# Kernel tuning notes

Measured on AMD Instinct MI355X. Metric: run time of the kernel, lower is better.

Reference implementation:

```python
import jax, jax.numpy as jnp
import numpy as np

B, N, F, D, TOPK, EXTRA = 32, 128, 10, 64, 20, 25
BN = B * N
EPS = 1e-5
SLOPE = 0.2  # GDN GraphLayer leaky_relu negative slope


def _cosine(a, b):
    na = jnp.maximum(jnp.linalg.norm(a, axis=-1), 1e-12)
    nb = jnp.maximum(jnp.linalg.norm(b, axis=-1), 1e-12)
    return (a @ b.T) / (na[:, None] * nb[None, :])


def _segment_softmax(logits, seg, num):
    m = jax.ops.segment_max(logits, seg, num_segments=num)
    m = jnp.where(jnp.isfinite(m), m, 0.0)  # empty segments
    e = jnp.exp(logits - m[seg])
    s = jax.ops.segment_sum(e, seg, num_segments=num)
    return e / jnp.maximum(s[seg], 1e-12)


def setup_inputs() -> dict:
    key = jax.random.key(0)
    ks = jax.random.split(key, 12)
    r = lambda i, shape, s=1.0: jax.random.normal(ks[i], shape, dtype=jnp.float32) * s
    return dict(
        data=r(0, (B, N, F)),
        emb=r(1, (N, D)) * 0.3,                       # nn.Embedding(node_num, dim)
        W1=r(2, (F, D)) * (1.0 / np.sqrt(F)),         # GraphLayer lin
        att_i1=r(3, (2 * D,)) * 0.1,                  # att on concat(h, emb)
        att_j1=r(4, (2 * D,)) * 0.1,
        bias1=jnp.zeros((D,), jnp.float32),
        bn1_g=jnp.ones((D,), jnp.float32),
        bn1_b=jnp.zeros((D,), jnp.float32),
        P=r(5, (BN, BN)) * (1.0 / np.sqrt(BN)),       # extra_pram
        W2=r(6, (D, D)) * (1.0 / np.sqrt(D)),         # GraphLayer1 lin
        att_i2=r(7, (D,)) * 0.1,
        att_j2=r(8, (D,)) * 0.1,
        bias2=jnp.zeros((D,), jnp.float32),
        bnO_g=jnp.ones((D,), jnp.float32),
        bnO_b=jnp.zeros((D,), jnp.float32),
        W_out=r(9, (D, 1)) * (1.0 / np.sqrt(D)),      # OutLayer Linear(dim,1)
        b_out=jnp.zeros((1,), jnp.float32),
        org_edge_index=jnp.zeros((2, 2), jnp.int32),  # dead arg in original forward
    )


def _forward(data, emb, W1, att_i1, att_j1, bias1, bn1_g, bn1_b, P, W2,
             att_i2, att_j2, bias2, bnO_g, bnO_b, W_out, b_out):
    x = data.reshape(BN, F)

    # ---- learned top-k graph from detached embedding cosine similarity ----
    w = jax.lax.stop_gradient(emb)              # weights_arr = detach()
    cos = _cosine(w, w)                         # [N, N]
    topv, topi = jax.lax.top_k(cos, TOPK)       # [N, TOPK]
    cos_w = jnp.tile(topv.reshape(-1), B)       # [B*N*TOPK]
    src0 = topi.reshape(-1)                     # gated_j (source)
    dst0 = jnp.repeat(jnp.arange(N), TOPK)      # gated_i (target)
    offs = jnp.repeat(jnp.arange(B) * N, N * TOPK)
    src = jnp.tile(src0, B) + offs
    dst = jnp.tile(dst0, B) + offs

    # ---- GraphLayer (GAT-style with embedding keys, edge weight = cos) ----
    all_emb = jnp.tile(emb, (B, 1))             # [BN, D]
    h = x @ W1                                  # [BN, D]
    kf = jnp.concatenate([h, all_emb], axis=-1) # [BN, 2D]
    si, sj = kf @ att_i1, kf @ att_j1           # [BN]
    score = jax.nn.leaky_relu(si[dst] + sj[src], SLOPE) * cos_w
    alpha = _segment_softmax(score, dst, BN)
    agg = jax.ops.segment_sum(h[src] * alpha[:, None], dst, num_segments=BN) + bias1
    mu, var = agg.mean(0), agg.var(0)           # BatchNorm1d (batch stats)
    gcn = jax.nn.relu(bn1_g * (agg - mu) / jnp.sqrt(var + EPS) + bn1_b)

    # ---- extra-feature branch (always taken: P is [BN, BN]) ----
    ef = P.T @ gcn                              # (gcn_out.T @ P).T
    g = jnp.concatenate([gcn, ef], axis=0)      # [2BN, D]
    cos2 = _cosine(g, g)                        # [2BN, 2BN]
    topv2, topi2 = jax.lax.top_k(cos2, EXTRA)
    corrs = topv2[:BN].reshape(-1)              # [BN*EXTRA]
    src2 = jnp.repeat(jnp.arange(BN), EXTRA)    # extra_i = edge_index[0] (source)
    dst2 = topi2[:BN].reshape(-1)               # extra_j = edge_index[1] (target)

    # ---- GraphLayer1 (no embedding keys, no BN in GNNLayer1.forward) ----
    h2 = g @ W2                                 # [2BN, D]
    s2 = jax.nn.leaky_relu((h2 @ att_i2)[dst2] + (h2 @ att_j2)[src2], SLOPE) * corrs
    alpha2 = _segment_softmax(s2, dst2, 2 * BN)
    agg2 = jax.ops.segment_sum(h2[src2] * alpha2[:, None], dst2, num_segments=2 * BN) + bias2
    gcn2 = jax.nn.relu(agg2)[:BN]

    # ---- output head: mul by embedding, BN over channels, Linear(D,1) ----
    x3 = gcn2.reshape(B, N, D) * emb[None]      # [B, N, D]
    mu2, var2 = x3.mean((0, 1)), x3.var((0, 1)) # BatchNorm1d over channel D
    x4 = jax.nn.relu(bnO_g * (x3 - mu2) / jnp.sqrt(var2 + EPS) + bnO_b)
    out = x4 @ W_out + b_out                    # [B, N, 1]; dropout = identity (eval)
    return out.reshape(-1, N)                   # [B, N]


def reference(data, emb, W1, att_i1, att_j1, bias1, bn1_g, bn1_b, P, W2,
              att_i2, att_j2, bias2, bnO_g, bnO_b, W_out, b_out, org_edge_index):
    # org_edge_index is dead in the original forward (only cached, never consumed)
    return _forward(data, emb, W1, att_i1, att_j1, bias1, bn1_g, bn1_b, P, W2,
                    att_i2, att_j2, bias2, bnO_g, bnO_b, W_out, b_out)
```

## Files before the change

### kernel.cpp

```cpp
#include <hip/hip_runtime.h>
#include <hip/hip_bf16.h>
#include <math.h>

#define DEV __device__ __forceinline__

constexpr int Bb   = 32;
constexpr int Nn   = 128;
constexpr int Ff   = 10;
constexpr int Dd   = 64;
constexpr int TOPK = 20;
constexpr int EXTRA= 25;
constexpr int BN   = 4096;
constexpr int TBN  = 8192;
constexpr int RC   = 16;
constexpr int CAND_CAP = 1024;
constexpr float EPS   = 1e-5f;
constexpr float SLOPE = 0.2f;

typedef __attribute__((ext_vector_type(8))) short bf16x8;
typedef __attribute__((ext_vector_type(4))) float f32x4;

DEV unsigned int fenc(float f){
  unsigned int b = __float_as_uint(f);
  return (b & 0x80000000u) ? ~b : (b | 0x80000000u);
}
DEV float fdec(unsigned int u){
  unsigned int b = (u & 0x80000000u) ? (u & 0x7FFFFFFFu) : ~u;
  return __uint_as_float(b);
}

DEV unsigned short f2bf(float f){
  unsigned u = __float_as_uint(f);
  u += 0x7FFFu + ((u >> 16) & 1u);
  return (unsigned short)(u >> 16);
}
DEV float bf2f(unsigned short h){
  return __uint_as_float(((unsigned)h) << 16);
}

__global__ void k_zero(float* __restrict__ p, int n){
  int i = blockIdx.x*256 + threadIdx.x;
  if(i < n) p[i] = 0.f;
}

__global__ void k_emb_norm(const float* __restrict__ emb, float* __restrict__ norms){
  int i = blockIdx.x, d = threadIdx.x;
  float v = emb[i*Dd + d];
  float s = v*v;
  for(int o=32;o>0;o>>=1) s += __shfl_down(s, o, 64);
  if(d==0) norms[i] = fmaxf(sqrtf(s), 1e-12f);
}

__global__ void k_emb_topk(const float* __restrict__ emb, const float* __restrict__ norms,
                           float* __restrict__ topv, int* __restrict__ topi){
  __shared__ float se[Dd];
  __shared__ float sc[Nn];
  __shared__ float rv[Nn];
  __shared__ int   ri[Nn];
  int i = blockIdx.x, t = threadIdx.x;
  if(t < Dd) se[t] = emb[i*Dd + t];
  __syncthreads();
  float dot = 0.f;
  for(int d=0; d<Dd; d++) dot += se[d]*emb[t*Dd + d];
  sc[t] = dot/(norms[i]*norms[t]);
  __syncthreads();
  for(int k=0; k<TOPK; k++){
    rv[t] = sc[t]; ri[t] = t; __syncthreads();
    for(int o=Nn/2; o>0; o>>=1){
      if(t < o){
        float v2 = rv[t+o]; int i2 = ri[t+o];
        if(v2 > rv[t] || (v2 == rv[t] && i2 < ri[t])){ rv[t]=v2; ri[t]=i2; }
      }
      __syncthreads();
    }
    if(t==0){
      topv[i*TOPK + k] = rv[0];
      topi[i*TOPK + k] = ri[0];
      sc[ri[0]] = -INFINITY;
    }
    __syncthreads();
  }
}

__global__ void k_h1(const float* __restrict__ data, const float* __restrict__ emb,
                     const float* __restrict__ W1, const float* __restrict__ ai1,
                     const float* __restrict__ aj1,
                     float* __restrict__ h, float* __restrict__ si, float* __restrict__ sj){
  int r = blockIdx.x, d = threadIdx.x;
  int node = r & (Nn-1);
  __shared__ float xr[Ff];
  if(d < Ff) xr[d] = data[r*Ff + d];
  __syncthreads();
  float hv = 0.f;
  #pragma unroll
  for(int f=0; f<Ff; f++) hv += xr[f]*W1[f*Dd + d];
  h[r*Dd + d] = hv;
  float e = emb[node*Dd + d];
  float a = hv*ai1[d] + e*ai1[Dd + d];
  float b = hv*aj1[d] + e*aj1[Dd + d];
  for(int o=32;o>0;o>>=1){ a += __shfl_down(a,o,64); b += __shfl_down(b,o,64); }
  if(d==0){ si[r] = a; sj[r] = b; }
}

__global__ void k_agg1(const float* __restrict__ h, const float* __restrict__ si,
                       const float* __restrict__ sj, const float* __restrict__ topv,
                       const int* __restrict__ topi, const float* __restrict__ bias1,
                       float* __restrict__ agg){
  int r = blockIdx.x, d = threadIdx.x;
  int b = r >> 7, node = r & (Nn-1);
  __shared__ float sal[TOPK];
  __shared__ int   ssrc[TOPK];
  if(d < TOPK){
    int s = b*Nn + topi[node*TOPK + d];
    float sc = si[r] + sj[s];
    sc = sc >= 0.f ? sc : SLOPE*sc;
    sal[d] = sc * topv[node*TOPK + d];
    ssrc[d] = s;
  }
  __syncthreads();
  float m = -INFINITY;
  #pragma unroll
  for(int k=0;k<TOPK;k++) m = fmaxf(m, sal[k]);
  float al[TOPK]; float ssum = 0.f;
  #pragma unroll
  for(int k=0;k<TOPK;k++){ al[k] = expf(sal[k]-m); ssum += al[k]; }
  float inv = 1.0f/fmaxf(ssum, 1e-12f);
  float acc = 0.f;
  #pragma unroll
  for(int k=0;k<TOPK;k++) acc += al[k]*inv*h[ssrc[k]*Dd + d];
  agg[r*Dd + d] = acc + bias1[d];
}

__global__ void k_colstats(const float* __restrict__ x, float* __restrict__ mu, float* __restrict__ var){
  int c = blockIdx.x, t = threadIdx.x;
  float s = 0.f, s2 = 0.f;
  for(int r=t; r<BN; r+=256){ float v = x[r*Dd + c]; s += v; s2 += v*v; }
  __shared__ float ls[256], ls2[256];
  ls[t]=s; ls2[t]=s2; __syncthreads();
  for(int o=128;o>0;o>>=1){
    if(t<o){ ls[t]+=ls[t+o]; ls2[t]+=ls2[t+o]; }
    __syncthreads();
  }
  if(t==0){ float m = ls[0]/BN; mu[c]=m; var[c]=ls2[0]/BN - m*m; }
}

__global__ void k_bnrelu1(const float* __restrict__ agg, const float* __restrict__ mu,
                          const float* __restrict__ var, const float* __restrict__ gamma,
                          const float* __restrict__ beta, float* __restrict__ g){
  int idx = blockIdx.x*256 + threadIdx.x;
  int c = idx & (Dd-1);
  float v = agg[idx];
  float y = gamma[c]*(v - mu[c])/sqrtf(var[c]+EPS) + beta[c];
  g[idx] = fmaxf(y, 0.f);
}

__global__ __launch_bounds__(256) void k_ef1(const float* __restrict__ P, const float* __restrict__ gcn,
                                             float* __restrict__ part){
  __shared__ float Pt[16*64];
  __shared__ float Gt[16*64];
  int t = threadIdx.x;
  int jbase = blockIdx.x*64;
  int r0 = blockIdx.y*256;
  int row = t >> 4, col4 = (t & 15)*4;
  int tr = t >> 4, tc = t & 15;
  float acc[4][4] = {};
  for(int step=0; step<16; step++){
    int r = r0 + step*16;
    float4 pv = *(const float4*)&P[(size_t)(r+row)*BN + jbase + col4];
    float4 gv = *(const float4*)&gcn[(r+row)*Dd + col4];
    __syncthreads();
    *(float4*)&Pt[row*64 + col4] = pv;
    *(float4*)&Gt[row*64 + col4] = gv;
    __syncthreads();
    #pragma unroll
    for(int rr=0; rr<16; rr++){
      float4 pa = *(float4*)&Pt[rr*64 + tr*4];
      float4 gb = *(float4*)&Gt[rr*64 + tc*4];
      float pav[4] = {pa.x, pa.y, pa.z, pa.w};
      float gbv[4] = {gb.x, gb.y, gb.z, gb.w};
      #pragma unroll
      for(int a=0;a<4;a++)
        #pragma unroll
        for(int b=0;b<4;b++) acc[a][b] += pav[a]*gbv[b];
    }
  }
  float* dst = part + ((size_t)blockIdx.y*BN + jbase)*Dd;
  #pragma unroll
  for(int a=0;a<4;a++){
    float4 v = make_float4(acc[a][0],acc[a][1],acc[a][2],acc[a][3]);
    *(float4*)&dst[(tr*4+a)*Dd + tc*4] = v;
  }
}

__global__ void k_ef2(const float* __restrict__ part, float* __restrict__ ef){
  int i = blockIdx.x*256 + threadIdx.x;
  float4 s = make_float4(0.f,0.f,0.f,0.f);
  #pragma unroll
  for(int c=0;c<RC;c++){
    float4 v = *(const float4*)&part[(size_t)c*BN*Dd + (size_t)i*4];
    s.x += v.x; s.y += v.y; s.z += v.z; s.w += v.w;
  }
  *(float4*)&ef[(size_t)i*4] = s;
}

__global__ void k_gn(const float* __restrict__ x,
                     unsigned short* __restrict__ gh,
                     unsigned short* __restrict__ gm,
                     unsigned short* __restrict__ gl){
  int r = blockIdx.x, d = threadIdx.x;
  float v = x[(size_t)r*Dd + d];
  float s = v*v;
  for(int o=32;o>0;o>>=1) s += __shfl_down(s, o, 64);
  s = __shfl(s, 0, 64);
  float inv = 1.0f/fmaxf(sqrtf(s), 1e-12f);
  float vn = v*inv;
  unsigned short h = f2bf(vn);
  float r1 = vn - bf2f(h);
  unsigned short m = f2bf(r1);
  float r2 = r1 - bf2f(m);
  unsigned short l = f2bf(r2);
  size_t idx = (size_t)r*Dd + d;
  gh[idx] = h; gm[idx] = m; gl[idx] = l;
}

__global__ __launch_bounds__(256) void k_sgemm(const unsigned short* __restrict__ gh,
                                               const unsigned short* __restrict__ gm,
                                               const unsigned short* __restrict__ gl,
                                               int rbase, float* __restrict__ S){
  int t = threadIdx.x;
  int w = t >> 6, l = t & 63;
  int lr = l & 15;
  int kq = l >> 4;
  int ctile = blockIdx.x*128;
  int rtile0 = rbase + blockIdx.y*128 + w*32;

  bf16x8 ah[2][2], am[2][2], alo[2][2];
  #pragma unroll
  for(int m=0;m<2;m++){
    size_t rowoff = (size_t)(rtile0 + m*16 + lr)*Dd;
    #pragma unroll
    for(int kh=0;kh<2;kh++){
      size_t off = rowoff + kh*32 + kq*8;
      ah[m][kh]  = *(const bf16x8*)(gh + off);
      am[m][kh]  = *(const bf16x8*)(gm + off);
      alo[m][kh] = *(const bf16x8*)(gl + off);
    }
  }
  f32x4 acc[2][8];
  #pragma unroll
  for(int m=0;m<2;m++)
    #pragma unroll
    for(int n=0;n<8;n++)
      acc[m][n] = (f32x4){0.f,0.f,0.f,0.f};

  #pragma unroll
  for(int n=0;n<8;n++){
    size_t coloff = (size_t)(ctile + n*16 + lr)*Dd;
    bf16x8 bh0 = *(const bf16x8*)(gh + coloff + kq*8);
    bf16x8 bh1 = *(const bf16x8*)(gh + coloff + 32 + kq*8);
    bf16x8 bm0 = *(const bf16x8*)(gm + coloff + kq*8);
    bf16x8 bm1 = *(const bf16x8*)(gm + coloff + 32 + kq*8);
    bf16x8 bl0 = *(const bf16x8*)(gl + coloff + kq*8);
    bf16x8 bl1 = *(const bf16x8*)(gl + coloff + 32 + kq*8);
    #pragma unroll
    for(int m=0;m<2;m++){
      f32x4 c = acc[m][n];
      c = __builtin_amdgcn_mfma_f32_16x16x32_bf16(ah[m][0], bh0, c, 0,0,0);
      c = __builtin_amdgcn_mfma_f32_16x16x32_bf16(ah[m][1], bh1, c, 0,0,0);
      c = __builtin_amdgcn_mfma_f32_16x16x32_bf16(ah[m][0], bm0, c, 0,0,0);
      c = __builtin_amdgcn_mfma_f32_16x16x32_bf16(ah[m][1], bm1, c, 0,0,0);
      c = __builtin_amdgcn_mfma_f32_16x16x32_bf16(am[m][0], bh0, c, 0,0,0);
      c = __builtin_amdgcn_mfma_f32_16x16x32_bf16(am[m][1], bh1, c, 0,0,0);
      c = __builtin_amdgcn_mfma_f32_16x16x32_bf16(ah[m][0], bl0, c, 0,0,0);
      c = __builtin_amdgcn_mfma_f32_16x16x32_bf16(ah[m][1], bl1, c, 0,0,0);
      c = __builtin_amdgcn_mfma_f32_16x16x32_bf16(alo[m][0], bh0, c, 0,0,0);
      c = __builtin_amdgcn_mfma_f32_16x16x32_bf16(alo[m][1], bh1, c, 0,0,0);
      c = __builtin_amdgcn_mfma_f32_16x16x32_bf16(am[m][0], bm0, c, 0,0,0);
      c = __builtin_amdgcn_mfma_f32_16x16x32_bf16(am[m][1], bm1, c, 0,0,0);
      acc[m][n] = c;
    }
  }

  int rloc = blockIdx.y*128 + w*32;
  #pragma unroll
  for(int m=0;m<2;m++){
    #pragma unroll
    for(int j=0;j<4;j++){
      int row = rloc + m*16 + kq*4 + j;
      #pragma unroll
      for(int n=0;n<8;n++){
        S[(size_t)row*TBN + ctile + n*16 + lr] = acc[m][n][j];
      }
    }
  }
}

__global__ __launch_bounds__(256) void k_radix(const float* __restrict__ S, int rbase,
                                               float* __restrict__ topv2, int* __restrict__ topi2){
  __shared__ unsigned hist[4096];
  __shared__ unsigned wtot[4];
  __shared__ unsigned candE[CAND_CAP];
  __shared__ unsigned short candC[CAND_CAP];
  __shared__ unsigned bc_bin, bc_need, bc_cnt, bc_c;
  int t = threadIdx.x;
  int lane = t & 63, wid = t >> 6;
  int r = blockIdx.x;
  const float* src = S + (size_t)r*TBN;
  int col0 = t*32;
  unsigned enc[32];
  #pragma unroll
  for(int j=0;j<8;j++){
    float4 v = *(const float4*)&src[col0 + j*4];
    enc[j*4+0]=fenc(v.x); enc[j*4+1]=fenc(v.y); enc[j*4+2]=fenc(v.z); enc[j*4+3]=fenc(v.w);
  }
  #pragma unroll
  for(int j=0;j<16;j++) hist[t*16 + j] = 0u;
  __syncthreads();
  #pragma unroll
  for(int j=0;j<32;j++) atomicAdd(&hist[enc[j] >> 20], 1u);
  __syncthreads();
  unsigned lsum = 0u;
  #pragma unroll
  for(int j=0;j<16;j++) lsum += hist[t*16 + j];
  unsigned v = lsum;
  #pragma unroll
  for(int o=1;o<64;o<<=1){
    unsigned u = (unsigned)__shfl_down((int)v, o, 64);
    if(lane + o < 64) v += u;
  }
  if(lane == 0) wtot[wid] = v;
  __syncthreads();
  unsigned cross = 0u;
  #pragma unroll
  for(int w2=0;w2<4;w2++) if(w2 > wid) cross += wtot[w2];
  unsigned Tinc = v + cross;
  unsigned above = Tinc - lsum;
  unsigned run = above;
  #pragma unroll
  for(int b=15;b>=0;b--){
    unsigned prev = run;
    run += hist[t*16 + b];
    if(run >= EXTRA && prev < EXTRA){ bc_bin = (unsigned)(t*16 + b); bc_need = EXTRA - prev; }
  }
  if(t==0){ bc_cnt = 0u; bc_c = 0u; }
  __syncthreads();
  unsigned pivotBin = bc_bin, needIn = bc_need;
  int gr = rbase + r;
  #pragma unroll
  for(int j=0;j<32;j++){
    unsigned e = enc[j];
    unsigned bin = e >> 20;
    if(bin > pivotBin){
      unsigned s = atomicAdd(&bc_cnt, 1u);
      topv2[gr*EXTRA + s] = fdec(e);
      topi2[gr*EXTRA + s] = col0 + j;
    } else if(bin == pivotBin){
      unsigned ci = atomicAdd(&bc_c, 1u);
      if(ci < CAND_CAP){ candE[ci] = e; candC[ci] = (unsigned short)(col0 + j); }
    }
  }
  __syncthreads();
  unsigned c = bc_c;
  if(c <= CAND_CAP){
    for(unsigned i=t; i<c; i+=256){
      unsigned ei = candE[i]; unsigned coli = candC[i];
      unsigned rank = 0;
      for(unsigned j2=0;j2<c;j2++){
        unsigned ej = candE[j2];
        rank += (ej > ei) || (ej == ei && candC[j2] < coli);
      }
      if(rank < needIn){
        unsigned s = atomicAdd(&bc_cnt, 1u);
        topv2[gr*EXTRA + s] = fdec(ei);
        topi2[gr*EXTRA + s] = (int)coli;
      }
    }
  } else {
    unsigned* h256  = hist;
    unsigned* scanb = hist + 1024;
    unsigned prefix = pivotBin;
    unsigned need = needIn;
    const int shifts[3] = {12, 4, 0};
    const unsigned masks[3] = {255u, 255u, 15u};
    const int nbins[3] = {256, 256, 16};
    for(int p=0;p<3;p++){
      int sh = shifts[p]; unsigned mk = masks[p]; int nb = nbins[p];
      if(t < nb) h256[t] = 0u;
      __syncthreads();
      #pragma unroll
      for(int j=0;j<32;j++){
        unsigned e = enc[j];
        int pshift = (p==0)? 20 : (p==1? 12 : 4);
        if((e >> pshift) == prefix) atomicAdd(&h256[(e>>sh)&mk], 1u);
      }
      __syncthreads();
      unsigned vv = (t < nb) ? h256[t] : 0u;
      for(int o=1;o<nb;o<<=1){
        if(t < nb) scanb[t] = vv;
        __syncthreads();
        if(t < nb && t+o < nb) vv += scanb[t+o];
        __syncthreads();
      }
      if(t < nb) scanb[t] = vv;
      __syncthreads();
      if(t < nb){
        unsigned nxt = (t < nb-1) ? scanb[t+1] : 0u;
        if(vv >= need && nxt < need){ bc_bin = (prefix << ((p==2)?4:8)) | (unsigned)t; bc_need = need - nxt; }
      }
      __syncthreads();
      prefix = bc_bin; need = bc_need;
      __syncthreads();
    }
    unsigned pivotEnc = prefix;
    unsigned needTies = need;
    unsigned tie_local = 0u;
    #pragma unroll
    for(int j=0;j<32;j++){
      unsigned e = enc[j];
      if((e >> 20) == pivotBin){
        if(e > pivotEnc){
          unsigned s = atomicAdd(&bc_cnt, 1u);
          topv2[gr*EXTRA + s] = fdec(e);
          topi2[gr*EXTRA + s] = col0 + j;
        } else if(e == pivotEnc) tie_local++;
      }
    }
    unsigned iv = tie_local;
    for(int o=1;o<256;o<<=1){
      scanb[t] = iv; __syncthreads();
      if(t >= o) iv += scanb[t-o];
      __syncthreads();
    }
    unsigned rank = iv - tie_local;
    #pragma unroll
    for(int j=0;j<32;j++){
      unsigned e = enc[j];
      if(e == pivotEnc && (e >> 20) == pivotBin){
        if(rank < needTies){
          unsigned s = atomicAdd(&bc_cnt, 1u);
          topv2[gr*EXTRA + s] = fdec(e);
          topi2[gr*EXTRA + s] = col0 + j;
        }
        rank++;
      }
    }
  }
}

__global__ void k_h2(const float* __restrict__ g, const float* __restrict__ W2,
                     const float* __restrict__ ai2w, const float* __restrict__ aj2w,
                     float* __restrict__ h2, float* __restrict__ a2i, float* __restrict__ a2j){
  int r = blockIdx.x, d = threadIdx.x;
  __shared__ float gr[Dd];
  gr[d] = g[(size_t)r*Dd + d];
  __syncthreads();
  float hv = 0.f;
  #pragma unroll
  for(int k=0;k<Dd;k++) hv += gr[k]*W2[k*Dd + d];
  h2[(size_t)r*Dd + d] = hv;
  float a = hv*ai2w[d];
  float b = hv*aj2w[d];
  for(int o=32;o>0;o>>=1){ a += __shfl_down(a,o,64); b += __shfl_down(b,o,64); }
  if(d==0){ a2i[r]=a; a2j[r]=b; }
}

__global__ void k_s2(const float* __restrict__ a2i, const float* __restrict__ a2j,
                     const float* __restrict__ topv2, const int* __restrict__ topi2,
                     float* __restrict__ s2, unsigned int* __restrict__ segmax){
  int e = blockIdx.x*256 + threadIdx.x;
  if(e >= BN*EXTRA) return;
  int r = e/EXTRA;
  int dst = topi2[e];
  float sc = a2i[dst] + a2j[r];
  sc = sc >= 0.f ? sc : SLOPE*sc;
  sc *= topv2[e];
  s2[e] = sc;
  atomicMax(&segmax[dst], fenc(sc));
}

__global__ void k_e2(const float* __restrict__ s2, const int* __restrict__ topi2,
                     const unsigned int* __restrict__ segmax,
                     float* __restrict__ e2, float* __restrict__ ssum){
  int e = blockIdx.x*256 + threadIdx.x;
  if(e >= BN*EXTRA) return;
  int dst = topi2[e];
  float m = fdec(segmax[dst]);
  float v = expf(s2[e] - m);
  e2[e] = v;
  atomicAdd(&ssum[dst], v);
}

__global__ void k_scat(const float* __restrict__ e2, const float* __restrict__ ssum,
                       const int* __restrict__ topi2, const float* __restrict__ h2,
                       float* __restrict__ agg2){
  int idx = blockIdx.x*256 + threadIdx.x;
  int e = idx >> 6, d = idx & 63;
  int dst = topi2[e];
  int src = e/EXTRA;
  float alpha = e2[e]/fmaxf(ssum[dst], 1e-12f);
  atomicAdd(&agg2[(size_t)dst*Dd + d], alpha*h2[(size_t)src*Dd + d]);
}

__global__ void k_headstats(const float* __restrict__ agg2, const float* __restrict__ bias2,
                            const float* __restrict__ emb, float* __restrict__ mu2, float* __restrict__ var2){
  int c = blockIdx.x, t = threadIdx.x;
  float bc = bias2[c];
  float s = 0.f, s2 = 0.f;
  for(int r=t; r<BN; r+=256){
    float v = fmaxf(agg2[(size_t)r*Dd + c] + bc, 0.f) * emb[(r & (Nn-1))*Dd + c];
    s += v; s2 += v*v;
  }
  __shared__ float ls[256], ls2[256];
  ls[t]=s; ls2[t]=s2; __syncthreads();
  for(int o=128;o>0;o>>=1){
    if(t<o){ ls[t]+=ls[t+o]; ls2[t]+=ls2[t+o]; }
    __syncthreads();
  }
  if(t==0){ float m=ls[0]/BN; mu2[c]=m; var2[c]=ls2[0]/BN - m*m; }
}

__global__ void k_out(const float* __restrict__ agg2, const float* __restrict__ bias2,
                      const float* __restrict__ emb, const float* __restrict__ mu2,
                      const float* __restrict__ var2, const float* __restrict__ gO,
                      const float* __restrict__ bO, const float* __restrict__ Wout,
                      const float* __restrict__ bout, float* __restrict__ out){
  int r = blockIdx.x, d = threadIdx.x;
  float v = fmaxf(agg2[(size_t)r*Dd + d] + bias2[d], 0.f) * emb[(r & (Nn-1))*Dd + d];
  float y = gO[d]*(v - mu2[d])/sqrtf(var2[d]+EPS) + bO[d];
  y = fmaxf(y, 0.f)*Wout[d];
  for(int o=32;o>0;o>>=1) y += __shfl_down(y, o, 64);
  if(d==0) out[r] = y + bout[0];
}

extern "C" void kernel_launch(void* const* d_in, const int* in_sizes, int n_in,
                              void* d_out, int out_size, void* d_ws, size_t ws_size,
                              hipStream_t stream){
  const float* data  = (const float*)d_in[0];
  const float* emb   = (const float*)d_in[1];
  const float* W1    = (const float*)d_in[2];
  const float* ai1   = (const float*)d_in[3];
  const float* aj1   = (const float*)d_in[4];
  const float* bias1 = (const float*)d_in[5];
  const float* bn1g  = (const float*)d_in[6];
  const float* bn1b  = (const float*)d_in[7];
  const float* P     = (const float*)d_in[8];
  const float* W2    = (const float*)d_in[9];
  const float* ai2w  = (const float*)d_in[10];
  const float* aj2w  = (const float*)d_in[11];
  const float* bias2 = (const float*)d_in[12];
  const float* bnOg  = (const float*)d_in[13];
  const float* bnOb  = (const float*)d_in[14];
  const float* Wout  = (const float*)d_in[15];
  const float* bout  = (const float*)d_in[16];
  float* out = (float*)d_out;

  char* w = (char*)d_ws;
  auto alloc = [&](size_t nbytes)->char*{
    char* p = w; w += (nbytes + 255) & ~(size_t)255; return p;
  };
  float* norms1 = (float*)alloc(Nn*4);
  float* topv1  = (float*)alloc(Nn*TOPK*4);
  int*   topi1  = (int*)  alloc(Nn*TOPK*4);
  float* h      = (float*)alloc((size_t)BN*Dd*4);
  float* si     = (float*)alloc(BN*4);
  float* sj     = (float*)alloc(BN*4);
  float* agg1   = (float*)alloc((size_t)BN*Dd*4);
  float* mu1    = (float*)alloc(Dd*4);
  float* var1   = (float*)alloc(Dd*4);
  float* g      = (float*)alloc((size_t)TBN*Dd*4);
  unsigned short* gnh = (unsigned short*)alloc((size_t)TBN*Dd*2);
  unsigned short* gnm = (unsigned short*)alloc((size_t)TBN*Dd*2);
  unsigned short* gnl = (unsigned short*)alloc((size_t)TBN*Dd*2);
  float* topv2  = (float*)alloc((size_t)BN*EXTRA*4);
  int*   topi2  = (int*)  alloc((size_t)BN*EXTRA*4);
  float* h2     = (float*)alloc((size_t)TBN*Dd*4);
  float* a2i    = (float*)alloc(TBN*4);
  float* a2j    = (float*)alloc(TBN*4);
  float* s2     = (float*)alloc((size_t)BN*EXTRA*4);
  float* e2     = (float*)alloc((size_t)BN*EXTRA*4);
  float* zblock = (float*)alloc(((size_t)TBN*Dd + TBN + TBN)*4);
  float* agg2   = zblock;
  float* ssum   = zblock + (size_t)TBN*Dd;
  unsigned int* segmax = (unsigned int*)(ssum + TBN);
  float* mu2    = (float*)alloc(Dd*4);
  float* var2   = (float*)alloc(Dd*4);
  float* efpart = (float*)alloc((size_t)RC*BN*Dd*4);

  size_t used = (size_t)(w - (char*)d_ws);
  size_t rem  = ws_size > used ? ws_size - used : 0;
  int chunkRows = 4096;
  while(chunkRows > 128 && (size_t)chunkRows*TBN*4 > rem) chunkRows >>= 1;
  float* Schunk = (float*)alloc((size_t)chunkRows*TBN*4);

  k_emb_norm<<<Nn, 64, 0, stream>>>(emb, norms1);
  k_emb_topk<<<Nn, Nn, 0, stream>>>(emb, norms1, topv1, topi1);
  k_h1<<<BN, 64, 0, stream>>>(data, emb, W1, ai1, aj1, h, si, sj);
  k_agg1<<<BN, 64, 0, stream>>>(h, si, sj, topv1, topi1, bias1, agg1);
  k_colstats<<<Dd, 256, 0, stream>>>(agg1, mu1, var1);
  k_bnrelu1<<<(BN*Dd)/256, 256, 0, stream>>>(agg1, mu1, var1, bn1g, bn1b, g);

  k_ef1<<<dim3(64, RC), 256, 0, stream>>>(P, g, efpart);
  k_ef2<<<(BN*Dd/4)/256, 256, 0, stream>>>(efpart, g + (size_t)BN*Dd);

  k_gn<<<TBN, 64, 0, stream>>>(g, gnh, gnm, gnl);
  for(int rbase=0; rbase<BN; rbase+=chunkRows){
    k_sgemm<<<dim3(TBN/128, chunkRows/128), 256, 0, stream>>>(gnh, gnm, gnl, rbase, Schunk);
    k_radix<<<chunkRows, 256, 0, stream>>>(Schunk, rbase, topv2, topi2);
  }

  k_h2<<<TBN, 64, 0, stream>>>(g, W2, ai2w, aj2w, h2, a2i, a2j);
  k_zero<<<((TBN*Dd + 2*TBN) + 255)/256, 256, 0, stream>>>(zblock, TBN*Dd + 2*TBN);
  k_s2<<<(BN*EXTRA + 255)/256, 256, 0, stream>>>(a2i, a2j, topv2, topi2, s2, segmax);
  k_e2<<<(BN*EXTRA + 255)/256, 256, 0, stream>>>(s2, topi2, segmax, e2, ssum);
  k_scat<<<(BN*EXTRA*Dd)/256, 256, 0, stream>>>(e2, ssum, topi2, h2, agg2);

  k_headstats<<<Dd, 256, 0, stream>>>(agg2, bias2, emb, mu2, var2);
  k_out<<<BN, 64, 0, stream>>>(agg2, bias2, emb, mu2, var2, bnOg, bnOb, Wout, bout, out);
}
```

Before: 385.0 us.

## Prune top-k radix reads using per-tile maxima emitted by similarity GEMM

The similarity GEMM now writes, for each row, the maximum over every 128-column tile. The radix top-k kernel uses these to find the 25th-largest tile maximum and skips loading and histogramming any tile whose maximum falls below it. Such a tile cannot hold a top-25 value, so most of each S row no longer has to be read. The GEMM stores and radix loads also switch to nontemporal hints, and the later edge kernels gain a guard that drops edges whose destination index is out of range.

```diff
diff --git a/kernel.cpp b/kernel.cpp
--- a/kernel.cpp
+++ b/kernel.cpp
@@ -226,7 +226,8 @@
 __global__ __launch_bounds__(256) void k_sgemm(const unsigned short* __restrict__ gh,
                                                const unsigned short* __restrict__ gm,
                                                const unsigned short* __restrict__ gl,
-                                               int rbase, float* __restrict__ S){
+                                               int rbase, float* __restrict__ S,
+                                               float* __restrict__ Smax){
   int t = threadIdx.x;
   int w = t >> 6, l = t & 63;
   int lr = l & 15;
@@ -287,37 +288,67 @@
     #pragma unroll
     for(int j=0;j<4;j++){
       int row = rloc + m*16 + kq*4 + j;
+      float mx = acc[m][0][j];
       #pragma unroll
-      for(int n=0;n<8;n++){
-        S[(size_t)row*TBN + ctile + n*16 + lr] = acc[m][n][j];
-      }
-    }
-  }
-}
-
-__global__ __launch_bounds__(256) void k_radix(const float* __restrict__ S, int rbase,
+      for(int n=1;n<8;n++) mx = fmaxf(mx, acc[m][n][j]);
+      #pragma unroll
+      for(int o=1;o<16;o<<=1) mx = fmaxf(mx, __shfl_xor(mx, o, 64));
+      if(lr == 0) Smax[row*64 + blockIdx.x] = mx;
+      #pragma unroll
+      for(int n=0;n<8;n++)
+        __builtin_nontemporal_store(acc[m][n][j], &S[(size_t)row*TBN + ctile + n*16 + lr]);
+    }
+  }
+}
+
+__global__ __launch_bounds__(256) void k_radix(const float* __restrict__ S,
+                                               const float* __restrict__ Smax,
+                                               int rbase,
                                                float* __restrict__ topv2, int* __restrict__ topi2){
   __shared__ unsigned hist[4096];
   __shared__ unsigned wtot[4];
   __shared__ unsigned candE[CAND_CAP];
   __shared__ unsigned short candC[CAND_CAP];
   __shared__ unsigned bc_bin, bc_need, bc_cnt, bc_c;
+  __shared__ float stmax[64];
+  __shared__ float sLsh;
   int t = threadIdx.x;
   int lane = t & 63, wid = t >> 6;
   int r = blockIdx.x;
   const float* src = S + (size_t)r*TBN;
   int col0 = t*32;
+
+  if(t < 64) stmax[t] = Smax[r*64 + t];
+  #pragma unroll
+  for(int j=0;j<16;j++) hist[t*16 + j] = 0u;
+  if(t==0){ bc_cnt = 0u; bc_c = 0u; }
+  __syncthreads();
+  if(t < 64){
+    float mi = stmax[t];
+    int cnt = 0;
+    for(int j=0;j<64;j++){
+      float mj = stmax[j];
+      cnt += (mj > mi) || (mj == mi && j < t);
+    }
+    if(cnt == 24) sLsh = mi;
+  }
+  __syncthreads();
+  float L = sLsh;
+  bool skip = stmax[t >> 2] < L;
+
   unsigned enc[32];
-  #pragma unroll
-  for(int j=0;j<8;j++){
-    float4 v = *(const float4*)&src[col0 + j*4];
-    enc[j*4+0]=fenc(v.x); enc[j*4+1]=fenc(v.y); enc[j*4+2]=fenc(v.z); enc[j*4+3]=fenc(v.w);
-  }
-  #pragma unroll
-  for(int j=0;j<16;j++) hist[t*16 + j] = 0u;
-  __syncthreads();
-  #pragma unroll
-  for(int j=0;j<32;j++) atomicAdd(&hist[enc[j] >> 20], 1u);
+  if(!skip){
+    #pragma unroll
+    for(int j=0;j<8;j++){
+      f32x4 v = __builtin_nontemporal_load((const f32x4*)&src[col0 + j*4]);
+      enc[j*4+0]=fenc(v[0]); enc[j*4+1]=fenc(v[1]); enc[j*4+2]=fenc(v[2]); enc[j*4+3]=fenc(v[3]);
+    }
+    #pragma unroll
+    for(int j=0;j<32;j++) atomicAdd(&hist[enc[j] >> 20], 1u);
+  } else {
+    #pragma unroll
+    for(int j=0;j<32;j++) enc[j] = 0u;
+  }
   __syncthreads();
   unsigned lsum = 0u;
   #pragma unroll
@@ -342,7 +373,6 @@
     run += hist[t*16 + b];
     if(run >= EXTRA && prev < EXTRA){ bc_bin = (unsigned)(t*16 + b); bc_need = EXTRA - prev; }
   }
-  if(t==0){ bc_cnt = 0u; bc_c = 0u; }
   __syncthreads();
   unsigned pivotBin = bc_bin, needIn = bc_need;
   int gr = rbase + r;
@@ -471,6 +501,7 @@
   if(e >= BN*EXTRA) return;
   int r = e/EXTRA;
   int dst = topi2[e];
+  if(dst >= BN) return;
   float sc = a2i[dst] + a2j[r];
   sc = sc >= 0.f ? sc : SLOPE*sc;
   sc *= topv2[e];
@@ -484,6 +515,7 @@
   int e = blockIdx.x*256 + threadIdx.x;
   if(e >= BN*EXTRA) return;
   int dst = topi2[e];
+  if(dst >= BN) return;
   float m = fdec(segmax[dst]);
   float v = expf(s2[e] - m);
   e2[e] = v;
@@ -496,6 +528,7 @@
   int idx = blockIdx.x*256 + threadIdx.x;
   int e = idx >> 6, d = idx & 63;
   int dst = topi2[e];
+  if(dst >= BN) return;
   int src = e/EXTRA;
   float alpha = e2[e]/fmaxf(ssum[dst], 1e-12f);
   atomicAdd(&agg2[(size_t)dst*Dd + d], alpha*h2[(size_t)src*Dd + d]);
@@ -585,6 +618,7 @@
   float* mu2    = (float*)alloc(Dd*4);
   float* var2   = (float*)alloc(Dd*4);
   float* efpart = (float*)alloc((size_t)RC*BN*Dd*4);
+  float* SmaxB  = (float*)alloc((size_t)4096*64*4);
 
   size_t used = (size_t)(w - (char*)d_ws);
   size_t rem  = ws_size > used ? ws_size - used : 0;
@@ -604,8 +638,8 @@
 
   k_gn<<<TBN, 64, 0, stream>>>(g, gnh, gnm, gnl);
   for(int rbase=0; rbase<BN; rbase+=chunkRows){
-    k_sgemm<<<dim3(TBN/128, chunkRows/128), 256, 0, stream>>>(gnh, gnm, gnl, rbase, Schunk);
-    k_radix<<<chunkRows, 256, 0, stream>>>(Schunk, rbase, topv2, topi2);
+    k_sgemm<<<dim3(TBN/128, chunkRows/128), 256, 0, stream>>>(gnh, gnm, gnl, rbase, Schunk, SmaxB);
+    k_radix<<<chunkRows, 256, 0, stream>>>(Schunk, SmaxB, rbase, topv2, topi2);
   }
 
   k_h2<<<TBN, 64, 0, stream>>>(g, W2, ai2w, aj2w, h2, a2i, a2j);
```

Measured after the change: 378.4 us. Within noise of the previous version (-1.7%).

## Fuse similarity GEMM with top-k selection to avoid materializing the score matrix

Applied to the files above, without the earlier changes.

The chunked GEMM that wrote the full 4096x8192 similarity matrix, followed by a radix top-k pass, is replaced by one fused kernel. It first computes per-128-column tile row maxima and derives a per-row threshold from the 25th largest tile max. It then recomputes only the tiles that can contain top-k entries, collects candidates in shared memory, and ranks them per half-row. A merge kernel combines the two column halves, and a slow fallback kernel redoes rows whose candidate buffer overflowed. Edge kernels also skip destinations at or beyond BN, since those rows are never read. This trades a large global write and read plus extra kernel launches for recomputing the selected GEMM tiles, higher shared-memory use and the cost of the fallback path.

```diff
diff --git a/kernel.cpp b/kernel.cpp
--- a/kernel.cpp
+++ b/kernel.cpp
@@ -14,6 +14,8 @@
 constexpr int TBN  = 8192;
 constexpr int RC   = 16;
 constexpr int CAND_CAP = 1024;
+constexpr int CAP  = 448;
+constexpr int NT   = 32;
 constexpr float EPS   = 1e-5f;
 constexpr float SLOPE = 0.2f;
 
@@ -223,21 +225,61 @@
   gh[idx] = h; gm[idx] = m; gl[idx] = l;
 }
 
-__global__ __launch_bounds__(256) void k_sgemm(const unsigned short* __restrict__ gh,
+#define COMPUTE_TILE(CBASE) do{                                             \
+  _Pragma("unroll")                                                         \
+  for(int m=0;m<2;m++)                                                      \
+    _Pragma("unroll")                                                       \
+    for(int n=0;n<8;n++) acc[m][n] = (f32x4){0.f,0.f,0.f,0.f};              \
+  _Pragma("unroll")                                                         \
+  for(int n=0;n<8;n++){                                                     \
+    size_t coloff = (size_t)((CBASE) + n*16 + lr)*Dd;                       \
+    bf16x8 bh0 = *(const bf16x8*)(gh + coloff + kq*8);                      \
+    bf16x8 bh1 = *(const bf16x8*)(gh + coloff + 32 + kq*8);                 \
+    bf16x8 bm0 = *(const bf16x8*)(gm + coloff + kq*8);                      \
+    bf16x8 bm1 = *(const bf16x8*)(gm + coloff + 32 + kq*8);                 \
+    bf16x8 bl0 = *(const bf16x8*)(gl + coloff + kq*8);                      \
+    bf16x8 bl1 = *(const bf16x8*)(gl + coloff + 32 + kq*8);                 \
+    _Pragma("unroll")                                                       \
+    for(int m=0;m<2;m++){                                                   \
+      f32x4 cc = acc[m][n];                                                 \
+      cc = __builtin_amdgcn_mfma_f32_16x16x32_bf16(ah[m][0],  bh0, cc, 0,0,0); \
+      cc = __builtin_amdgcn_mfma_f32_16x16x32_bf16(ah[m][1],  bh1, cc, 0,0,0); \
+      cc = __builtin_amdgcn_mfma_f32_16x16x32_bf16(ah[m][0],  bm0, cc, 0,0,0); \
+      cc = __builtin_amdgcn_mfma_f32_16x16x32_bf16(ah[m][1],  bm1, cc, 0,0,0); \
+      cc = __builtin_amdgcn_mfma_f32_16x16x32_bf16(am[m][0],  bh0, cc, 0,0,0); \
+      cc = __builtin_amdgcn_mfma_f32_16x16x32_bf16(am[m][1],  bh1, cc, 0,0,0); \
+      cc = __builtin_amdgcn_mfma_f32_16x16x32_bf16(ah[m][0],  bl0, cc, 0,0,0); \
+      cc = __builtin_amdgcn_mfma_f32_16x16x32_bf16(ah[m][1],  bl1, cc, 0,0,0); \
+      cc = __builtin_amdgcn_mfma_f32_16x16x32_bf16(alo[m][0], bh0, cc, 0,0,0); \
+      cc = __builtin_amdgcn_mfma_f32_16x16x32_bf16(alo[m][1], bh1, cc, 0,0,0); \
+      cc = __builtin_amdgcn_mfma_f32_16x16x32_bf16(am[m][0],  bm0, cc, 0,0,0); \
+      cc = __builtin_amdgcn_mfma_f32_16x16x32_bf16(am[m][1],  bm1, cc, 0,0,0); \
+      acc[m][n] = cc;                                                       \
+    }                                                                       \
+  }                                                                         \
+}while(0)
+
+__global__ __launch_bounds__(256) void k_fused(const unsigned short* __restrict__ gh,
                                                const unsigned short* __restrict__ gm,
                                                const unsigned short* __restrict__ gl,
-                                               int rbase, float* __restrict__ S){
+                                               unsigned* __restrict__ splitV,
+                                               int* __restrict__ splitI,
+                                               int* __restrict__ flag){
+  __shared__ float tmax[32][NT];
+  __shared__ float Lsh[32];
+  __shared__ unsigned candn[32];
+  __shared__ unsigned candV[32][CAP];
+  __shared__ unsigned short candC[32][CAP];
   int t = threadIdx.x;
   int w = t >> 6, l = t & 63;
-  int lr = l & 15;
-  int kq = l >> 4;
-  int ctile = blockIdx.x*128;
-  int rtile0 = rbase + blockIdx.y*128 + w*32;
+  int lr = l & 15, kq = l >> 4;
+  int rloc0 = blockIdx.y*32;
+  int cbase0 = blockIdx.x*4096;
 
   bf16x8 ah[2][2], am[2][2], alo[2][2];
   #pragma unroll
   for(int m=0;m<2;m++){
-    size_t rowoff = (size_t)(rtile0 + m*16 + lr)*Dd;
+    size_t rowoff = (size_t)(rloc0 + m*16 + lr)*Dd;
     #pragma unroll
     for(int kh=0;kh<2;kh++){
       size_t off = rowoff + kh*32 + kq*8;
@@ -247,56 +289,122 @@
     }
   }
   f32x4 acc[2][8];
-  #pragma unroll
-  for(int m=0;m<2;m++)
-    #pragma unroll
-    for(int n=0;n<8;n++)
-      acc[m][n] = (f32x4){0.f,0.f,0.f,0.f};
-
-  #pragma unroll
-  for(int n=0;n<8;n++){
-    size_t coloff = (size_t)(ctile + n*16 + lr)*Dd;
-    bf16x8 bh0 = *(const bf16x8*)(gh + coloff + kq*8);
-    bf16x8 bh1 = *(const bf16x8*)(gh + coloff + 32 + kq*8);
-    bf16x8 bm0 = *(const bf16x8*)(gm + coloff + kq*8);
-    bf16x8 bm1 = *(const bf16x8*)(gm + coloff + 32 + kq*8);
-    bf16x8 bl0 = *(const bf16x8*)(gl + coloff + kq*8);
-    bf16x8 bl1 = *(const bf16x8*)(gl + coloff + 32 + kq*8);
+
+  for(int it=0; it<8; ++it){
+    int ct = it*4 + w;
+    COMPUTE_TILE(cbase0 + ct*128);
     #pragma unroll
     for(int m=0;m<2;m++){
-      f32x4 c = acc[m][n];
-      c = __builtin_amdgcn_mfma_f32_16x16x32_bf16(ah[m][0], bh0, c, 0,0,0);
-      c = __builtin_amdgcn_mfma_f32_16x16x32_bf16(ah[m][1], bh1, c, 0,0,0);
-      c = __builtin_amdgcn_mfma_f32_16x16x32_bf16(ah[m][0], bm0, c, 0,0,0);
-      c = __builtin_amdgcn_mfma_f32_16x16x32_bf16(ah[m][1], bm1, c, 0,0,0);
-      c = __builtin_amdgcn_mfma_f32_16x16x32_bf16(am[m][0], bh0, c, 0,0,0);
-      c = __builtin_amdgcn_mfma_f32_16x16x32_bf16(am[m][1], bh1, c, 0,0,0);
-      c = __builtin_amdgcn_mfma_f32_16x16x32_bf16(ah[m][0], bl0, c, 0,0,0);
-      c = __builtin_amdgcn_mfma_f32_16x16x32_bf16(ah[m][1], bl1, c, 0,0,0);
-      c = __builtin_amdgcn_mfma_f32_16x16x32_bf16(alo[m][0], bh0, c, 0,0,0);
-      c = __builtin_amdgcn_mfma_f32_16x16x32_bf16(alo[m][1], bh1, c, 0,0,0);
-      c = __builtin_amdgcn_mfma_f32_16x16x32_bf16(am[m][0], bm0, c, 0,0,0);
-      c = __builtin_amdgcn_mfma_f32_16x16x32_bf16(am[m][1], bm1, c, 0,0,0);
-      acc[m][n] = c;
-    }
-  }
-
-  int rloc = blockIdx.y*128 + w*32;
-  #pragma unroll
-  for(int m=0;m<2;m++){
+      #pragma unroll
+      for(int j=0;j<4;j++){
+        int row = m*16 + kq*4 + j;
+        float mx = acc[m][0][j];
+        #pragma unroll
+        for(int n=1;n<8;n++) mx = fmaxf(mx, acc[m][n][j]);
+        #pragma unroll
+        for(int o=1;o<16;o<<=1) mx = fmaxf(mx, __shfl_xor(mx, o, 64));
+        if(lr == 0) tmax[row][ct] = mx;
+      }
+    }
+  }
+  __syncthreads();
+
+  if(t < 32){
+    float Lr = 0.f;
+    for(int i=0;i<NT;i++){
+      float mi = tmax[t][i]; int cnt = 0;
+      for(int j=0;j<NT;j++){
+        float mj = tmax[t][j];
+        cnt += (mj > mi) || (mj == mi && j < i);
+      }
+      if(cnt == EXTRA-1) Lr = mi;
+    }
+    Lsh[t] = Lr;
+    candn[t] = 0u;
+  }
+  __syncthreads();
+
+  for(int it=0; it<8; ++it){
+    int ct = it*4 + w;
+    bool need = (l < 32) && (tmax[l][ct] >= Lsh[l]);
+    if(__ballot(need) == 0ull) continue;
+    COMPUTE_TILE(cbase0 + ct*128);
     #pragma unroll
-    for(int j=0;j<4;j++){
-      int row = rloc + m*16 + kq*4 + j;
+    for(int m=0;m<2;m++){
       #pragma unroll
-      for(int n=0;n<8;n++){
-        S[(size_t)row*TBN + ctile + n*16 + lr] = acc[m][n][j];
-      }
-    }
-  }
-}
-
-__global__ __launch_bounds__(256) void k_radix(const float* __restrict__ S, int rbase,
-                                               float* __restrict__ topv2, int* __restrict__ topi2){
+      for(int j=0;j<4;j++){
+        int row = m*16 + kq*4 + j;
+        float Lr = Lsh[row];
+        #pragma unroll
+        for(int n=0;n<8;n++){
+          float v = acc[m][n][j];
+          if(v >= Lr){
+            unsigned idx = atomicAdd(&candn[row], 1u);
+            if(idx < CAP){
+              candV[row][idx] = fenc(v);
+              candC[row][idx] = (unsigned short)(ct*128 + n*16 + lr);
+            }
+          }
+        }
+      }
+    }
+  }
+  __syncthreads();
+
+  int row = t >> 3, sub = t & 7;
+  unsigned cn = candn[row];
+  unsigned c  = cn < CAP ? cn : CAP;
+  int rg = rloc0 + row;
+  if(sub == 0 && cn > CAP) flag[rg] = 1;
+  for(unsigned i=sub; i<c; i+=8){
+    unsigned vi = candV[row][i]; unsigned ci = candC[row][i];
+    unsigned rank = 0;
+    for(unsigned j=0;j<c;j++){
+      unsigned vj = candV[row][j];
+      rank += (vj > vi) || (vj == vi && candC[row][j] < ci);
+    }
+    if(rank < EXTRA){
+      size_t o = (size_t)rg*(2*EXTRA) + blockIdx.x*EXTRA + rank;
+      splitV[o] = vi;
+      splitI[o] = cbase0 + (int)ci;
+    }
+  }
+}
+
+__global__ void k_merge(const unsigned* __restrict__ splitV, const int* __restrict__ splitI,
+                        float* __restrict__ topv2, int* __restrict__ topi2){
+  __shared__ unsigned mV[4][2*EXTRA];
+  __shared__ int mC[4][2*EXTRA];
+  int t = threadIdx.x;
+  int wid = t >> 6, lane = t & 63;
+  int row = blockIdx.x*4 + wid;
+  if(lane < 2*EXTRA){
+    mV[wid][lane] = splitV[(size_t)row*(2*EXTRA) + lane];
+    mC[wid][lane] = splitI[(size_t)row*(2*EXTRA) + lane];
+  }
+  __syncthreads();
+  if(lane < 2*EXTRA){
+    unsigned vi = mV[wid][lane]; int ci = mC[wid][lane];
+    int rank = 0;
+    for(int j=0;j<2*EXTRA;j++){
+      unsigned vj = mV[wid][j];
+      rank += (vj > vi) || (vj == vi && mC[wid][j] < ci);
+    }
+    if(rank < EXTRA){
+      topv2[row*EXTRA + rank] = fdec(vi);
+      topi2[row*EXTRA + rank] = ci;
+    }
+  }
+}
+
+__global__ __launch_bounds__(256) void k_fix(const unsigned short* __restrict__ gh,
+                                             const unsigned short* __restrict__ gm,
+                                             const unsigned short* __restrict__ gl,
+                                             const int* __restrict__ flag,
+                                             float* __restrict__ topv2, int* __restrict__ topi2){
+  int r = blockIdx.x;
+  if(flag[r] == 0) return;
+  __shared__ float vrow[Dd];
   __shared__ unsigned hist[4096];
   __shared__ unsigned wtot[4];
   __shared__ unsigned candE[CAND_CAP];
@@ -304,14 +412,18 @@
   __shared__ unsigned bc_bin, bc_need, bc_cnt, bc_c;
   int t = threadIdx.x;
   int lane = t & 63, wid = t >> 6;
-  int r = blockIdx.x;
-  const float* src = S + (size_t)r*TBN;
+  if(t < Dd) vrow[t] = bf2f(gh[(size_t)r*Dd+t]) + bf2f(gm[(size_t)r*Dd+t]) + bf2f(gl[(size_t)r*Dd+t]);
+  __syncthreads();
   int col0 = t*32;
   unsigned enc[32];
-  #pragma unroll
-  for(int j=0;j<8;j++){
-    float4 v = *(const float4*)&src[col0 + j*4];
-    enc[j*4+0]=fenc(v.x); enc[j*4+1]=fenc(v.y); enc[j*4+2]=fenc(v.z); enc[j*4+3]=fenc(v.w);
+  for(int j=0;j<32;j++){
+    int cidx = col0 + j;
+    const unsigned short* ph = gh + (size_t)cidx*Dd;
+    const unsigned short* pm = gm + (size_t)cidx*Dd;
+    const unsigned short* pl = gl + (size_t)cidx*Dd;
+    float s = 0.f;
+    for(int d=0; d<Dd; d++) s += vrow[d]*(bf2f(ph[d]) + bf2f(pm[d]) + bf2f(pl[d]));
+    enc[j] = fenc(s);
   }
   #pragma unroll
   for(int j=0;j<16;j++) hist[t*16 + j] = 0u;
@@ -345,7 +457,7 @@
   if(t==0){ bc_cnt = 0u; bc_c = 0u; }
   __syncthreads();
   unsigned pivotBin = bc_bin, needIn = bc_need;
-  int gr = rbase + r;
+  int gr = r;
   #pragma unroll
   for(int j=0;j<32;j++){
     unsigned e = enc[j];
@@ -471,6 +583,7 @@
   if(e >= BN*EXTRA) return;
   int r = e/EXTRA;
   int dst = topi2[e];
+  if(dst >= BN) return;
   float sc = a2i[dst] + a2j[r];
   sc = sc >= 0.f ? sc : SLOPE*sc;
   sc *= topv2[e];
@@ -484,6 +597,7 @@
   int e = blockIdx.x*256 + threadIdx.x;
   if(e >= BN*EXTRA) return;
   int dst = topi2[e];
+  if(dst >= BN) return;
   float m = fdec(segmax[dst]);
   float v = expf(s2[e] - m);
   e2[e] = v;
@@ -496,6 +610,7 @@
   int idx = blockIdx.x*256 + threadIdx.x;
   int e = idx >> 6, d = idx & 63;
   int dst = topi2[e];
+  if(dst >= BN) return;
   int src = e/EXTRA;
   float alpha = e2[e]/fmaxf(ssum[dst], 1e-12f);
   atomicAdd(&agg2[(size_t)dst*Dd + d], alpha*h2[(size_t)src*Dd + d]);
@@ -585,12 +700,9 @@
   float* mu2    = (float*)alloc(Dd*4);
   float* var2   = (float*)alloc(Dd*4);
   float* efpart = (float*)alloc((size_t)RC*BN*Dd*4);
-
-  size_t used = (size_t)(w - (char*)d_ws);
-  size_t rem  = ws_size > used ? ws_size - used : 0;
-  int chunkRows = 4096;
-  while(chunkRows > 128 && (size_t)chunkRows*TBN*4 > rem) chunkRows >>= 1;
-  float* Schunk = (float*)alloc((size_t)chunkRows*TBN*4);
+  unsigned* splitV = (unsigned*)alloc((size_t)BN*2*EXTRA*4);
+  int*      splitI = (int*)     alloc((size_t)BN*2*EXTRA*4);
+  int*      flagB  = (int*)     alloc((size_t)BN*4);
 
   k_emb_norm<<<Nn, 64, 0, stream>>>(emb, norms1);
   k_emb_topk<<<Nn, Nn, 0, stream>>>(emb, norms1, topv1, topi1);
@@ -603,10 +715,10 @@
   k_ef2<<<(BN*Dd/4)/256, 256, 0, stream>>>(efpart, g + (size_t)BN*Dd);
 
   k_gn<<<TBN, 64, 0, stream>>>(g, gnh, gnm, gnl);
-  for(int rbase=0; rbase<BN; rbase+=chunkRows){
-    k_sgemm<<<dim3(TBN/128, chunkRows/128), 256, 0, stream>>>(gnh, gnm, gnl, rbase, Schunk);
-    k_radix<<<chunkRows, 256, 0, stream>>>(Schunk, rbase, topv2, topi2);
-  }
+  k_zero<<<(BN + 255)/256, 256, 0, stream>>>((float*)flagB, BN);
+  k_fused<<<dim3(2, BN/32), 256, 0, stream>>>(gnh, gnm, gnl, splitV, splitI, flagB);
+  k_merge<<<BN/4, 256, 0, stream>>>(splitV, splitI, topv2, topi2);
+  k_fix<<<BN, 256, 0, stream>>>(gnh, gnm, gnl, flagB, topv2, topi2);
 
   k_h2<<<TBN, 64, 0, stream>>>(g, W2, ai2w, aj2w, h2, a2i, a2j);
   k_zero<<<((TBN*Dd + 2*TBN) + 255)/256, 256, 0, stream>>>(zblock, TBN*Dd + 2*TBN);
```

Measured after the change: 785.8 us. +104.1%, slower.
